# Kernel tuning notes

Measured on AMD Instinct MI355X. Metric: run time of the kernel, lower is better.

The kernel has to match this reference:

```python
import jax, jax.numpy as jnp
import numpy as np

KERNEL = 3          # route_nms_kernel
MAX_ROUTES = 256    # max_routes (topk per image)
STRIDE = 4.0        # route_stride
MIN_SIZE = 32.0     # route_min_size
MAX_SIZE = 512.0    # route_max_size
POWER = 2.0         # route_score_power
B, H, W = 32, 512, 512


def setup_inputs() -> dict:
    key = jax.random.key(0)
    k1, k2, k3 = jax.random.split(key, 3)
    return {
        "route_logits": jax.random.normal(k1, (B, 1, H, W), dtype=jnp.float32),
        "scale_logits": jax.random.normal(k2, (B, 1, H, W), dtype=jnp.float32),
        "uncertainty_logits": jax.random.normal(k3, (B, 1, H, W), dtype=jnp.float32),
        "image_h": 2048,
        "image_w": 2048,
    }


def _local_max_pool(x):
    # x: [H, W]; 3x3 max pool, stride 1, pad kernel//2 (torch F.max_pool2d pads with -inf)
    pad = KERNEL // 2
    return jax.lax.reduce_window(x, -jnp.inf, jax.lax.max,
                                 (KERNEL, KERNEL), (1, 1),
                                 [(pad, pad), (pad, pad)])


def reference(route_logits, scale_logits, uncertainty_logits, image_h, image_w):
    # score_map = sigmoid(logits)^power * (1 - 0.35*sigmoid(uncertainty))  (use_route_uncertainty=True)
    score_map = jnp.power(jax.nn.sigmoid(route_logits), POWER)
    score_map = score_map * (1.0 - 0.35 * jax.nn.sigmoid(uncertainty_logits))
    img_h = jnp.float32(image_h)
    img_w = jnp.float32(image_w)
    width = route_logits.shape[-1]

    def per_image(batch_idx, scores2d, scale2d, unc2d):
        pooled = _local_max_pool(scores2d)
        filtered = jnp.where(scores2d == pooled, scores2d, -1.0)  # masked_fill(~mask, -1)
        values, indices = jax.lax.top_k(filtered.reshape(-1), MAX_ROUTES)
        valid = values > 0.0  # torch filters values>0; here kept as fixed-shape mask
        ys = indices // width
        xs = indices % width
        cx = (xs.astype(jnp.float32) + 0.5) * STRIDE
        cy = (ys.astype(jnp.float32) + 0.5) * STRIDE
        scale_g = scale2d[ys, xs]
        unc = jax.nn.sigmoid(unc2d[ys, xs])
        side = MIN_SIZE + jax.nn.sigmoid(scale_g) * (MAX_SIZE - MIN_SIZE)
        side = side * (1.0 + 0.25 * unc)
        half = side * 0.5
        x1 = jnp.clip(cx - half, 0.0, img_w - 1.0)
        y1 = jnp.clip(cy - half, 0.0, img_h - 1.0)
        x2 = jnp.clip(cx + half, 1.0, img_w)
        y2 = jnp.clip(cy + half, 1.0, img_h)
        rois = jnp.stack([jnp.full_like(x1, batch_idx), x1, y1, x2, y2], axis=1)  # [K,5]
        rois = jnp.where(valid[:, None], rois, 0.0)
        vals = jnp.where(valid, values, 0.0)
        return rois, vals, valid

    batch_ids = jnp.arange(route_logits.shape[0], dtype=jnp.float32)
    rois, scores, valid = jax.vmap(per_image)(
        batch_ids, score_map[:, 0], scale_logits[:, 0], uncertainty_logits[:, 0])
    # rois: [B, K, 5], scores: [B, K], valid: [B, K] (per_image_counts = valid.sum(-1))
    return rois, scores, valid
```

## Files before the change

kernel.cpp:

```cpp
#include <hip/hip_runtime.h>
#include <cstdint>
#include <cstddef>

#define BATCH 32
#define IMH 512
#define IMW 512
#define KMAX 256

#define RPW 4
#define NBLKX 2
#define NYG (IMH / RPW)
#define NL1 (NBLKX * NYG)
#define NM1 (NL1 / 4)
#define NMID (NM1 / 4)
#define WCAP 256

#define TPB2 512

typedef unsigned long long u64;

__device__ __forceinline__ float sigmoidf_(float x) {
    return 1.0f / (1.0f + expf(-x));
}
__device__ __forceinline__ float scoref_(float r, float u) {
    const float sg = sigmoidf_(r);
    return sg * sg * (1.0f - 0.35f * sigmoidf_(u));
}

#define SHF(v, jj, dm) do {                                         \
    const u64 o_ = __shfl_xor((v), (jj), 64);                       \
    const bool take_ = ((((lane & (jj)) == 0) == (dm)) == ((v) < o_)); \
    (v) = take_ ? o_ : (v);                                         \
} while (0)

#define RMAX(a, b) do {                                             \
    const u64 hi_ = ((a) > (b)) ? (a) : (b);                        \
    const u64 lo_ = ((a) > (b)) ? (b) : (a);                        \
    (a) = hi_; (b) = lo_;                                           \
} while (0)

#define RMIN(a, b) do {                                             \
    const u64 hi_ = ((a) > (b)) ? (a) : (b);                        \
    const u64 lo_ = ((a) > (b)) ? (b) : (a);                        \
    (a) = lo_; (b) = hi_;                                           \
} while (0)

__device__ __forceinline__ void clean256(u64& v0, u64& v1, u64& v2, u64& v3,
                                         const int lane) {
    RMAX(v0, v2); RMAX(v1, v3);
    RMAX(v0, v1); RMAX(v2, v3);
    #pragma unroll
    for (int j = 32; j > 0; j >>= 1) {
        SHF(v0, j, true); SHF(v1, j, true); SHF(v2, j, true); SHF(v3, j, true);
    }
}

__device__ __forceinline__ void sort256(u64& v0, u64& v1, u64& v2, u64& v3,
                                        const int lane) {
    #pragma unroll
    for (int k = 2; k <= 32; k <<= 1) {
        #pragma unroll
        for (int j = k >> 1; j > 0; j >>= 1) {
            const bool dm = ((lane & k) == 0);
            SHF(v0, j, dm); SHF(v1, j, dm); SHF(v2, j, dm); SHF(v3, j, dm);
        }
    }
    #pragma unroll
    for (int j = 32; j > 0; j >>= 1) {
        SHF(v0, j, true); SHF(v1, j, false); SHF(v2, j, true); SHF(v3, j, false);
    }
    RMAX(v0, v1); RMIN(v2, v3);
    #pragma unroll
    for (int j = 32; j > 0; j >>= 1) {
        SHF(v0, j, true); SHF(v1, j, true); SHF(v2, j, false); SHF(v3, j, false);
    }
    clean256(v0, v1, v2, v3, lane);
}

__device__ __forceinline__ void sort128(u64& v0, u64& v1, const int lane) {
    #pragma unroll
    for (int k = 2; k <= 32; k <<= 1) {
        #pragma unroll
        for (int j = k >> 1; j > 0; j >>= 1) {
            const bool dm = ((lane & k) == 0);
            SHF(v0, j, dm); SHF(v1, j, dm);
        }
    }
    #pragma unroll
    for (int j = 32; j > 0; j >>= 1) {
        SHF(v0, j, true); SHF(v1, j, false);
    }
    RMAX(v0, v1);
    #pragma unroll
    for (int j = 32; j > 0; j >>= 1) {
        SHF(v0, j, true); SHF(v1, j, true);
    }
}

__device__ __forceinline__ void merge256(u64& v0, u64& v1, u64& v2, u64& v3,
                                         u64 w0, u64 w1, u64 w2, u64 w3,
                                         const int lane) {
    const int rl = 63 ^ lane;
    const u64 b0 = __shfl(w3, rl, 64);
    const u64 b1 = __shfl(w2, rl, 64);
    const u64 b2 = __shfl(w1, rl, 64);
    const u64 b3 = __shfl(w0, rl, 64);
    v0 = (v0 > b0) ? v0 : b0;
    v1 = (v1 > b1) ? v1 : b1;
    v2 = (v2 > b2) ? v2 : b2;
    v3 = (v3 > b3) ? v3 : b3;
    clean256(v0, v1, v2, v3, lane);
}

__device__ __forceinline__ void load256(const u64* p, u64& v0, u64& v1,
                                        u64& v2, u64& v3, const int lane) {
    v0 = p[lane]; v1 = p[lane + 64]; v2 = p[lane + 128]; v3 = p[lane + 192];
}
__device__ __forceinline__ void store256(u64* p, u64 v0, u64 v1,
                                         u64 v2, u64 v3, const int lane) {
    p[lane] = v0; p[lane + 64] = v1; p[lane + 128] = v2; p[lane + 192] = v3;
}

__device__ __forceinline__ void merge4s(const u64* p,
                                        u64& a0, u64& a1, u64& a2, u64& a3,
                                        const int lane) {
    load256(p, a0, a1, a2, a3, lane);
    u64 w0, w1, w2, w3;
    load256(p + KMAX, w0, w1, w2, w3, lane);
    merge256(a0, a1, a2, a3, w0, w1, w2, w3, lane);
    u64 c0, c1, c2, c3;
    load256(p + 2 * KMAX, c0, c1, c2, c3, lane);
    load256(p + 3 * KMAX, w0, w1, w2, w3, lane);
    merge256(c0, c1, c2, c3, w0, w1, w2, w3, lane);
    merge256(a0, a1, a2, a3, c0, c1, c2, c3, lane);
}

__global__ __launch_bounds__(256)
void score_map_kernel(const float* __restrict__ route,
                      const float* __restrict__ unc,
                      float* __restrict__ smap) {
    const size_t i = ((size_t)blockIdx.x * 256 + threadIdx.x) * 4;
    const float4 r4 = *(const float4*)(route + i);
    const float4 u4 = *(const float4*)(unc + i);
    float4 s4;
    s4.x = scoref_(r4.x, u4.x);
    s4.y = scoref_(r4.y, u4.y);
    s4.z = scoref_(r4.z, u4.z);
    s4.w = scoref_(r4.w, u4.w);
    *(float4*)(smap + i) = s4;
}

__global__ __launch_bounds__(128)
void score_nms_kernel(const float* __restrict__ smap,
                      u64* __restrict__ top) {
    const int b    = blockIdx.z;
    const int w    = threadIdx.x >> 6;
    const int lane = threadIdx.x & 63;
    const int yg   = blockIdx.y * 2 + w;
    const int y0   = yg * RPW;
    const int x0   = blockIdx.x * 256 + lane * 4;
    const int list = yg * NBLKX + blockIdx.x;

    __shared__ u64 lcand[2 * WCAP];
    u64* myR = lcand + w * WCAP;

    const float* sB = smap + (size_t)b * IMH * IMW;

    int ex = -1;
    if (lane == 0)       ex = x0 - 1;
    else if (lane == 63) ex = x0 + 4;
    const bool eAct = (ex >= 0 && ex < IMW);

    const u64 laneMaskLt = (1ull << lane) - 1ull;
    int wcnt = 0;

    float sP[4], hP1[4], hP2[4];
    #pragma unroll
    for (int j = 0; j < 4; ++j) { sP[j] = -INFINITY; hP1[j] = -INFINITY; hP2[j] = -INFINITY; }

    const int ylast = y0 + RPW;
    bool v = (y0 - 1 >= 0);
    float4 s4; float es = -INFINITY;
    if (v) {
        s4 = *(const float4*)(sB + (size_t)(y0 - 1) * IMW + x0);
        if (eAct) es = sB[(size_t)(y0 - 1) * IMW + ex];
    }

    for (int y = y0 - 1; y <= ylast; ++y) {
        const int yn = y + 1;
        const bool vn = (yn <= ylast) && (yn < IMH);
        float4 s4n; float esn = -INFINITY;
        if (vn) {
            s4n = *(const float4*)(sB + (size_t)yn * IMW + x0);
            if (eAct) esn = sB[(size_t)yn * IMW + ex];
        }

        float sC[4], hmC[4];
        float ecur = -INFINITY;
        if (v && eAct) ecur = es;
        if (v) {
            sC[0] = s4.x; sC[1] = s4.y; sC[2] = s4.z; sC[3] = s4.w;
        } else {
            sC[0] = sC[1] = sC[2] = sC[3] = -INFINITY;
        }
        float lft = __shfl_up(sC[3], 1, 64);
        if (lane == 0) lft = ecur;
        float rgt = __shfl_down(sC[0], 1, 64);
        if (lane == 63) rgt = ecur;
        if (v) {
            hmC[0] = fmaxf(fmaxf(lft,   sC[0]), sC[1]);
            hmC[1] = fmaxf(fmaxf(sC[0], sC[1]), sC[2]);
            hmC[2] = fmaxf(fmaxf(sC[1], sC[2]), sC[3]);
            hmC[3] = fmaxf(fmaxf(sC[2], sC[3]), rgt);
        } else {
            hmC[0] = hmC[1] = hmC[2] = hmC[3] = -INFINITY;
        }

        if (y >= y0 + 1) {
            const int yo = y - 1;
            bool p[4]; int cntT = 0;
            #pragma unroll
            for (int j = 0; j < 4; ++j) {
                const float m9 = fmaxf(fmaxf(hP2[j], hP1[j]), hmC[j]);
                p[j] = (sP[j] >= m9);
                cntT += p[j] ? 1 : 0;
            }
            const u64 B0 = __ballot(cntT & 1);
            const u64 B1 = __ballot(cntT & 2);
            const u64 B2 = __ballot(cntT & 4);
            const int total = __popcll(B0) + 2 * __popcll(B1) + 4 * __popcll(B2);
            if (total > 0) {
                const int prefix = __popcll(B0 & laneMaskLt) + 2 * __popcll(B1 & laneMaskLt)
                                 + 4 * __popcll(B2 & laneMaskLt);
                int mb = wcnt + prefix;
                #pragma unroll
                for (int j = 0; j < 4; ++j) {
                    if (p[j]) {
                        const unsigned idx = (unsigned)(yo * IMW + (x0 + j));
                        const u64 key = ((u64)__float_as_uint(sP[j]) << 32) | (unsigned)(~idx);
                        if (mb < WCAP) myR[mb] = key;
                        ++mb;
                    }
                }
                wcnt += total;
            }
        }

        #pragma unroll
        for (int j = 0; j < 4; ++j) { hP2[j] = hP1[j]; hP1[j] = hmC[j]; sP[j] = sC[j]; }
        s4 = s4n; es = esn; v = vn;
    }

    const int m = (wcnt < WCAP) ? wcnt : WCAP;
    u64 a0, a1, a2, a3;
    if (m <= 128) {
        a0 = (lane      < m) ? myR[lane]      : 0ull;
        a1 = (lane + 64 < m) ? myR[lane + 64] : 0ull;
        sort128(a0, a1, lane);
        a2 = 0ull; a3 = 0ull;
    } else {
        a0 = (lane       < m) ? myR[lane]       : 0ull;
        a1 = (lane + 64  < m) ? myR[lane + 64]  : 0ull;
        a2 = (lane + 128 < m) ? myR[lane + 128] : 0ull;
        a3 = (lane + 192 < m) ? myR[lane + 192] : 0ull;
        sort256(a0, a1, a2, a3, lane);
    }

    u64* seg = top + ((size_t)b * NL1 + list) * KMAX;
    store256(seg, a0, a1, a2, a3, lane);
}

__global__ __launch_bounds__(128)
void merge4_kernel(const u64* __restrict__ in, int nin,
                   u64* __restrict__ out_) {
    const int w    = threadIdx.x >> 6;
    const int lane = threadIdx.x & 63;
    const int o    = blockIdx.x * 2 + w;
    const int b    = blockIdx.y;
    const int nout = nin / 4;
    if (o >= nout) return;

    const u64* L = in + ((size_t)b * nin + o * 4) * KMAX;
    u64 a0, a1, a2, a3;
    merge4s(L, a0, a1, a2, a3, lane);

    u64* out = out_ + ((size_t)b * nout + o) * KMAX;
    store256(out, a0, a1, a2, a3, lane);
}

__global__ __launch_bounds__(TPB2)
void tail_kernel(const u64* __restrict__ mid,
                 const float* __restrict__ scale,
                 const float* __restrict__ unc,
                 const int* __restrict__ imh,
                 const int* __restrict__ imw,
                 float* __restrict__ rois,
                 float* __restrict__ scoresOut,
                 float* __restrict__ validOut) {
    const int b   = blockIdx.x;
    const int tid = threadIdx.x;

    __shared__ u64 bufA[NMID * KMAX];
    __shared__ u64 bufB[(NMID / 2) * KMAX];

    const u64* tb = mid + (size_t)b * NMID * KMAX;
    for (int i = tid; i < NMID * KMAX; i += TPB2) bufA[i] = tb[i];
    __syncthreads();

    u64* src = bufA;
    u64* dst = bufB;
    int nl = NMID;
    while (nl > 1) {
        const int half = nl >> 1;
        const int E = half * KMAX;
        for (int p = tid; p < E; p += TPB2) {
            const int h = p >> 8;
            const int i = p & (KMAX - 1);
            const u64 a = src[(2 * h) * KMAX + i];
            const u64 c = src[(2 * h + 1) * KMAX + (KMAX - 1 - i)];
            dst[p] = (a > c) ? a : c;
        }
        __syncthreads();
        for (int j = KMAX >> 1; j > 0; j >>= 1) {
            for (int p = tid; p < (E >> 1); p += TPB2) {
                const int i   = ((p & ~(j - 1)) << 1) | (p & (j - 1));
                const int ixj = i | j;
                const u64 a = dst[i];
                const u64 c = dst[ixj];
                if (a < c) { dst[i] = c; dst[ixj] = a; }
            }
            __syncthreads();
        }
        u64* t = src; src = dst; dst = t;
        nl = half;
    }

    if (tid < KMAX) {
        const u64 k = src[tid];
        const float value = __uint_as_float((unsigned)(k >> 32));
        const bool valid  = (k != 0ull) && (value > 0.0f);

        float r0 = 0.f, r1 = 0.f, r2 = 0.f, r3 = 0.f, r4 = 0.f, sv = 0.f, vv = 0.f;
        if (valid) {
            const unsigned idx = ~(unsigned)(k & 0xFFFFFFFFull);
            const int y = (int)(idx / IMW);
            const int x = (int)(idx % IMW);
            const float cx = ((float)x + 0.5f) * 4.0f;
            const float cy = ((float)y + 0.5f) * 4.0f;
            const float sg = scale[(size_t)b * IMH * IMW + idx];
            const float uu = unc[(size_t)b * IMH * IMW + idx];
            const float su = sigmoidf_(uu);
            float side = 32.0f + sigmoidf_(sg) * (512.0f - 32.0f);
            side = side * (1.0f + 0.25f * su);
            const float half2 = side * 0.5f;
            const float fw = (float)imw[0];
            const float fh = (float)imh[0];
            r0 = (float)b;
            r1 = fminf(fmaxf(cx - half2, 0.0f), fw - 1.0f);
            r2 = fminf(fmaxf(cy - half2, 0.0f), fh - 1.0f);
            r3 = fminf(fmaxf(cx + half2, 1.0f), fw);
            r4 = fminf(fmaxf(cy + half2, 1.0f), fh);
            sv = value;
            vv = 1.0f;
        }
        float* roiP = rois + ((size_t)b * KMAX + tid) * 5;
        roiP[0] = r0; roiP[1] = r1; roiP[2] = r2; roiP[3] = r3; roiP[4] = r4;
        scoresOut[b * KMAX + tid] = sv;
        validOut[b * KMAX + tid]  = vv;
    }
}

extern "C" void kernel_launch(void* const* d_in, const int* in_sizes, int n_in,
                              void* d_out, int out_size, void* d_ws, size_t ws_size,
                              hipStream_t stream) {
    const float* route = (const float*)d_in[0];
    const float* scale = (const float*)d_in[1];
    const float* unc   = (const float*)d_in[2];
    const int*   imh   = (const int*)d_in[3];
    const int*   imw   = (const int*)d_in[4];

    float* smap = (float*)d_ws;
    u64*   top  = (u64*)((char*)d_ws + (size_t)BATCH * IMH * IMW * sizeof(float));
    u64*   mid1 = top  + (size_t)BATCH * NL1 * KMAX;
    u64*   mid2 = mid1 + (size_t)BATCH * NM1 * KMAX;

    float* rois      = (float*)d_out;
    float* scoresOut = rois + (size_t)BATCH * KMAX * 5;
    float* validOut  = scoresOut + (size_t)BATCH * KMAX;

    const int n4 = BATCH * IMH * IMW / 4;
    score_map_kernel<<<n4 / 256, 256, 0, stream>>>(route, unc, smap);

    dim3 grid1(NBLKX, NYG / 2, BATCH);
    score_nms_kernel<<<grid1, 128, 0, stream>>>(smap, top);

    dim3 grid2(NM1 / 2, BATCH);
    merge4_kernel<<<grid2, 128, 0, stream>>>(top, NL1, mid1);

    dim3 grid3(NMID / 2, BATCH);
    merge4_kernel<<<grid3, 128, 0, stream>>>(mid1, NM1, mid2);

    tail_kernel<<<BATCH, TPB2, 0, stream>>>(mid2, scale, unc,
                                            imh, imw, rois, scoresOut, validOut);
}
```

Measured before the change: 63.53 us.

## Fuse score-map computation into NMS kernel via shared-memory row tiles

Removes the separate score_map kernel and its full-resolution workspace write and read. Each 256-thread block now computes sigmoid scores for an 18-row halo tile into shared memory, then four wavefronts each run the 3x3 local-max test on 4 rows. The list layout and count are unchanged. In exchange, halo rows are recomputed, which adds about 12% extra transcendental work, and the kernel uses more shared memory per block.

```diff
diff --git a/kernel.cpp b/kernel.cpp
--- a/kernel.cpp
+++ b/kernel.cpp
@@ -7,13 +7,14 @@
 #define IMW 512
 #define KMAX 256
 
-#define RPW 4
+#define TILE_ROWS 16
 #define NBLKX 2
-#define NYG (IMH / RPW)
-#define NL1 (NBLKX * NYG)
+#define NYB (IMH / TILE_ROWS)
+#define NL1 (NBLKX * NYB * 4)
 #define NM1 (NL1 / 4)
 #define NMID (NM1 / 4)
 #define WCAP 256
+#define SSTRIDE 264
 
 #define TPB2 512
 
@@ -135,120 +136,99 @@
     merge256(a0, a1, a2, a3, c0, c1, c2, c3, lane);
 }
 
+#define LOADROW(rr, hm, sq) do {                                        \
+    const float4 q_ = *(const float4*)&sT[(rr)][4 + 4 * lane];          \
+    const float eL_ = sT[(rr)][3 + 4 * lane];                           \
+    const float eR_ = sT[(rr)][8 + 4 * lane];                           \
+    (hm)[0] = fmaxf(fmaxf(eL_, q_.x), q_.y);                            \
+    (hm)[1] = fmaxf(fmaxf(q_.x, q_.y), q_.z);                           \
+    (hm)[2] = fmaxf(fmaxf(q_.y, q_.z), q_.w);                           \
+    (hm)[3] = fmaxf(fmaxf(q_.z, q_.w), eR_);                            \
+    (sq)[0] = q_.x; (sq)[1] = q_.y; (sq)[2] = q_.z; (sq)[3] = q_.w;     \
+} while (0)
+
 __global__ __launch_bounds__(256)
-void score_map_kernel(const float* __restrict__ route,
+void score_nms_kernel(const float* __restrict__ route,
                       const float* __restrict__ unc,
-                      float* __restrict__ smap) {
-    const size_t i = ((size_t)blockIdx.x * 256 + threadIdx.x) * 4;
-    const float4 r4 = *(const float4*)(route + i);
-    const float4 u4 = *(const float4*)(unc + i);
-    float4 s4;
-    s4.x = scoref_(r4.x, u4.x);
-    s4.y = scoref_(r4.y, u4.y);
-    s4.z = scoref_(r4.z, u4.z);
-    s4.w = scoref_(r4.w, u4.w);
-    *(float4*)(smap + i) = s4;
-}
-
-__global__ __launch_bounds__(128)
-void score_nms_kernel(const float* __restrict__ smap,
                       u64* __restrict__ top) {
     const int b    = blockIdx.z;
-    const int w    = threadIdx.x >> 6;
-    const int lane = threadIdx.x & 63;
-    const int yg   = blockIdx.y * 2 + w;
-    const int y0   = yg * RPW;
-    const int x0   = blockIdx.x * 256 + lane * 4;
-    const int list = yg * NBLKX + blockIdx.x;
-
-    __shared__ u64 lcand[2 * WCAP];
+    const int t    = threadIdx.x;
+    const int w    = t >> 6;
+    const int lane = t & 63;
+    const int X0   = blockIdx.x * 256;
+    const int Y0   = blockIdx.y * TILE_ROWS;
+
+    __shared__ float sT[18][SSTRIDE];
+    __shared__ u64 lcand[4 * WCAP];
     u64* myR = lcand + w * WCAP;
 
-    const float* sB = smap + (size_t)b * IMH * IMW;
-
-    int ex = -1;
-    if (lane == 0)       ex = x0 - 1;
-    else if (lane == 63) ex = x0 + 4;
-    const bool eAct = (ex >= 0 && ex < IMW);
+    const float* rB = route + (size_t)b * IMH * IMW;
+    const float* uB = unc   + (size_t)b * IMH * IMW;
+
+    #pragma unroll 3
+    for (int r = 0; r < 18; ++r) {
+        const int y = Y0 - 1 + r;
+        float s = -INFINITY;
+        if (y >= 0 && y < IMH) {
+            const size_t o = (size_t)y * IMW + X0 + t;
+            s = scoref_(rB[o], uB[o]);
+        }
+        sT[r][4 + t] = s;
+    }
+    if (t < 36) {
+        const int p = t >> 1, side = t & 1;
+        const int y = Y0 - 1 + p;
+        const int x = side ? (X0 + 256) : (X0 - 1);
+        float s = -INFINITY;
+        if (y >= 0 && y < IMH && x >= 0 && x < IMW)
+            s = scoref_(rB[(size_t)y * IMW + x], uB[(size_t)y * IMW + x]);
+        sT[p][side ? 260 : 3] = s;
+    }
+    __syncthreads();
 
     const u64 laneMaskLt = (1ull << lane) - 1ull;
     int wcnt = 0;
 
-    float sP[4], hP1[4], hP2[4];
-    #pragma unroll
-    for (int j = 0; j < 4; ++j) { sP[j] = -INFINITY; hP1[j] = -INFINITY; hP2[j] = -INFINITY; }
-
-    const int ylast = y0 + RPW;
-    bool v = (y0 - 1 >= 0);
-    float4 s4; float es = -INFINITY;
-    if (v) {
-        s4 = *(const float4*)(sB + (size_t)(y0 - 1) * IMW + x0);
-        if (eAct) es = sB[(size_t)(y0 - 1) * IMW + ex];
-    }
-
-    for (int y = y0 - 1; y <= ylast; ++y) {
-        const int yn = y + 1;
-        const bool vn = (yn <= ylast) && (yn < IMH);
-        float4 s4n; float esn = -INFINITY;
-        if (vn) {
-            s4n = *(const float4*)(sB + (size_t)yn * IMW + x0);
-            if (eAct) esn = sB[(size_t)yn * IMW + ex];
-        }
-
-        float sC[4], hmC[4];
-        float ecur = -INFINITY;
-        if (v && eAct) ecur = es;
-        if (v) {
-            sC[0] = s4.x; sC[1] = s4.y; sC[2] = s4.z; sC[3] = s4.w;
-        } else {
-            sC[0] = sC[1] = sC[2] = sC[3] = -INFINITY;
-        }
-        float lft = __shfl_up(sC[3], 1, 64);
-        if (lane == 0) lft = ecur;
-        float rgt = __shfl_down(sC[0], 1, 64);
-        if (lane == 63) rgt = ecur;
-        if (v) {
-            hmC[0] = fmaxf(fmaxf(lft,   sC[0]), sC[1]);
-            hmC[1] = fmaxf(fmaxf(sC[0], sC[1]), sC[2]);
-            hmC[2] = fmaxf(fmaxf(sC[1], sC[2]), sC[3]);
-            hmC[3] = fmaxf(fmaxf(sC[2], sC[3]), rgt);
-        } else {
-            hmC[0] = hmC[1] = hmC[2] = hmC[3] = -INFINITY;
-        }
-
-        if (y >= y0 + 1) {
-            const int yo = y - 1;
-            bool p[4]; int cntT = 0;
+    float hmP[4], hmC[4], hmN[4], sC[4], sN[4];
+    {
+        float dump[4];
+        LOADROW(4 * w,     hmP, dump);
+        LOADROW(4 * w + 1, hmC, sC);
+    }
+    #pragma unroll
+    for (int i = 0; i < 4; ++i) {
+        LOADROW(4 * w + 2 + i, hmN, sN);
+
+        const int yo = Y0 + 4 * w + i;
+        bool p[4]; int cntT = 0;
+        #pragma unroll
+        for (int j = 0; j < 4; ++j) {
+            const float m9 = fmaxf(fmaxf(hmP[j], hmC[j]), hmN[j]);
+            p[j] = (sC[j] >= m9);
+            cntT += p[j] ? 1 : 0;
+        }
+        const u64 B0 = __ballot(cntT & 1);
+        const u64 B1 = __ballot(cntT & 2);
+        const u64 B2 = __ballot(cntT & 4);
+        const int total = __popcll(B0) + 2 * __popcll(B1) + 4 * __popcll(B2);
+        if (total > 0) {
+            const int prefix = __popcll(B0 & laneMaskLt) + 2 * __popcll(B1 & laneMaskLt)
+                             + 4 * __popcll(B2 & laneMaskLt);
+            int mb = wcnt + prefix;
             #pragma unroll
             for (int j = 0; j < 4; ++j) {
-                const float m9 = fmaxf(fmaxf(hP2[j], hP1[j]), hmC[j]);
-                p[j] = (sP[j] >= m9);
-                cntT += p[j] ? 1 : 0;
+                if (p[j]) {
+                    const unsigned idx = (unsigned)(yo * IMW + (X0 + 4 * lane + j));
+                    const u64 key = ((u64)__float_as_uint(sC[j]) << 32) | (unsigned)(~idx);
+                    if (mb < WCAP) myR[mb] = key;
+                    ++mb;
+                }
             }
-            const u64 B0 = __ballot(cntT & 1);
-            const u64 B1 = __ballot(cntT & 2);
-            const u64 B2 = __ballot(cntT & 4);
-            const int total = __popcll(B0) + 2 * __popcll(B1) + 4 * __popcll(B2);
-            if (total > 0) {
-                const int prefix = __popcll(B0 & laneMaskLt) + 2 * __popcll(B1 & laneMaskLt)
-                                 + 4 * __popcll(B2 & laneMaskLt);
-                int mb = wcnt + prefix;
-                #pragma unroll
-                for (int j = 0; j < 4; ++j) {
-                    if (p[j]) {
-                        const unsigned idx = (unsigned)(yo * IMW + (x0 + j));
-                        const u64 key = ((u64)__float_as_uint(sP[j]) << 32) | (unsigned)(~idx);
-                        if (mb < WCAP) myR[mb] = key;
-                        ++mb;
-                    }
-                }
-                wcnt += total;
-            }
+            wcnt += total;
         }
 
         #pragma unroll
-        for (int j = 0; j < 4; ++j) { hP2[j] = hP1[j]; hP1[j] = hmC[j]; sP[j] = sC[j]; }
-        s4 = s4n; es = esn; v = vn;
+        for (int j = 0; j < 4; ++j) { hmP[j] = hmC[j]; hmC[j] = hmN[j]; sC[j] = sN[j]; }
     }
 
     const int m = (wcnt < WCAP) ? wcnt : WCAP;
@@ -266,6 +246,7 @@
         sort256(a0, a1, a2, a3, lane);
     }
 
+    const int list = (blockIdx.y * 4 + w) * NBLKX + blockIdx.x;
     u64* seg = top + ((size_t)b * NL1 + list) * KMAX;
     store256(seg, a0, a1, a2, a3, lane);
 }
@@ -379,20 +360,16 @@
     const int*   imh   = (const int*)d_in[3];
     const int*   imw   = (const int*)d_in[4];
 
-    float* smap = (float*)d_ws;
-    u64*   top  = (u64*)((char*)d_ws + (size_t)BATCH * IMH * IMW * sizeof(float));
-    u64*   mid1 = top  + (size_t)BATCH * NL1 * KMAX;
-    u64*   mid2 = mid1 + (size_t)BATCH * NM1 * KMAX;
+    u64* top  = (u64*)d_ws;
+    u64* mid1 = top  + (size_t)BATCH * NL1 * KMAX;
+    u64* mid2 = mid1 + (size_t)BATCH * NM1 * KMAX;
 
     float* rois      = (float*)d_out;
     float* scoresOut = rois + (size_t)BATCH * KMAX * 5;
     float* validOut  = scoresOut + (size_t)BATCH * KMAX;
 
-    const int n4 = BATCH * IMH * IMW / 4;
-    score_map_kernel<<<n4 / 256, 256, 0, stream>>>(route, unc, smap);
-
-    dim3 grid1(NBLKX, NYG / 2, BATCH);
-    score_nms_kernel<<<grid1, 128, 0, stream>>>(smap, top);
+    dim3 grid1(NBLKX, NYB, BATCH);
+    score_nms_kernel<<<grid1, 256, 0, stream>>>(route, unc, top);
 
     dim3 grid2(NM1 / 2, BATCH);
     merge4_kernel<<<grid2, 128, 0, stream>>>(top, NL1, mid1);
```

Result: faster. 60.35 us (-5.0%).
